# Kernel tuning notes

Hardware: AMD Instinct MI355X
Metric: run time of the kernel (lower is better)

The kernel has to match this reference:

```python
import jax, jax.numpy as jnp
import numpy as np

NIBBLE_SHIFTS = jnp.arange(8, dtype=jnp.int32) * 4


def _unpack_int4(packed):
    # packed: [..., P] int32 -> [..., P*8] int32 values in [0, 15]
    vals = (packed[..., None] >> NIBBLE_SHIFTS) & 0xF
    return vals.reshape(*packed.shape[:-1], packed.shape[-1] * 8)


def setup_inputs() -> dict:
    key = jax.random.key(0)
    k1, k2, k3, k4, k5, k6 = jax.random.split(key, 6)
    M, K, N, G = 4096, 4096, 11008, 128
    inp = jax.random.normal(k1, (M, K), dtype=jnp.float32)
    qweight = jax.random.randint(k2, (K, N // 8), 0, 2147483647, dtype=jnp.int32)
    woq_scales = jax.random.uniform(k3, (K // G, N), dtype=jnp.float32)
    woq_qzeros = jax.random.randint(k4, (K // G, N // 8), 0, 2147483647, dtype=jnp.int32)
    woq_bias = jax.random.normal(k5, (N,), dtype=jnp.float32)
    mul = jax.random.normal(k6, (M, N), dtype=jnp.float32)
    return {"inp": inp, "qweight": qweight, "woq_scales": woq_scales,
            "woq_qzeros": woq_qzeros, "woq_bias": woq_bias, "mul": mul,
            "group_size": G}


def reference(inp, qweight, woq_scales, woq_qzeros, woq_bias, mul, group_size):
    K = qweight.shape[0]
    # dequantize int4 weights: w = (q - z) * scale, per group of `group_size` K-rows
    w_int = _unpack_int4(qweight).astype(jnp.float32)            # [K, N]
    z_int = _unpack_int4(woq_qzeros).astype(jnp.float32)         # [K/G, N]
    zeros_full = jnp.repeat(z_int, group_size, axis=0)           # [K, N]
    scales_full = jnp.repeat(woq_scales, group_size, axis=0)     # [K, N]
    w = (w_int - zeros_full) * scales_full                       # [K, N]
    woq_out = inp @ w + woq_bias                                 # [M, N]
    return jax.nn.silu(woq_out) * mul
```

## Files before the change

### kernel.cpp

```cpp
#include <hip/hip_runtime.h>
#include <hip/hip_bf16.h>

typedef __attribute__((ext_vector_type(8))) short short8;
typedef __attribute__((ext_vector_type(4))) short short4v;
typedef __attribute__((ext_vector_type(4))) float float4v;

__device__ __forceinline__ short f2bf(float f) {
  union { float f; unsigned u; } v; v.f = f;
  unsigned r = v.u + 0x7fffu + ((v.u >> 16) & 1u);
  return (short)(r >> 16);
}

typedef const __attribute__((address_space(1))) unsigned int* as1_u32p;
typedef __attribute__((address_space(3))) unsigned int* as3_u32p;

__device__ __forceinline__ void gl_lds16(const void* g, void* l) {
  __builtin_amdgcn_global_load_lds((as1_u32p)g, (as3_u32p)l, 16, 0, 0);
}

__global__ __launch_bounds__(256, 4)
void prep_kernel(const int* __restrict__ qw,
                 const float* __restrict__ scales,
                 const int* __restrict__ qzeros,
                 short* __restrict__ Bt,
                 const float* __restrict__ inp,
                 short* __restrict__ Abf,
                 int K, int N, int G, int nDq, long long nA)
{
  constexpr int KP = 72;
  __shared__ short Ls[256 * KP];

  if ((int)blockIdx.x >= nDq) {
    const long long i =
        (((long long)blockIdx.x - nDq) * blockDim.x + threadIdx.x) * 8;
    if (i >= nA) return;
    const float4v a = *(const float4v*)(inp + i);
    const float4v b = *(const float4v*)(inp + i + 4);
    short8 h;
    h[0] = f2bf(a[0]); h[1] = f2bf(a[1]); h[2] = f2bf(a[2]); h[3] = f2bf(a[3]);
    h[4] = f2bf(b[0]); h[5] = f2bf(b[1]); h[6] = f2bf(b[2]); h[7] = f2bf(b[3]);
    *(short8*)(Abf + i) = h;
    return;
  }

  const int KB  = K >> 6;
  const int N8  = N >> 3;
  const int k0  = ((int)blockIdx.x % KB) * 64;
  const int nb  = (int)blockIdx.x / KB;
  const int n0  = nb * 256;
  const int n80 = nb * 32;
  const int g   = k0 / G;
  const int t   = threadIdx.x;
  const int kloc = t >> 3;
  const int w4   = (t & 7) * 4;

  const int4 z4 = *(const int4*)(qzeros + (size_t)g * N8 + n80 + w4);
  const int za[4] = {z4.x, z4.y, z4.z, z4.w};
  float sc[32];
  #pragma unroll
  for (int ii = 0; ii < 8; ++ii)
    *(float4v*)(sc + ii * 4) =
        *(const float4v*)(scales + (size_t)g * N + n0 + w4 * 8 + ii * 4);

  #pragma unroll
  for (int kh = 0; kh < 2; ++kh) {
    const int k = kloc + kh * 32;
    const int4 q4 = *(const int4*)(qw + (size_t)(k0 + k) * N8 + n80 + w4);
    const int qa[4] = {q4.x, q4.y, q4.z, q4.w};
    #pragma unroll
    for (int ii = 0; ii < 4; ++ii) {
      #pragma unroll
      for (int j = 0; j < 8; ++j) {
        const float z = (float)((za[ii] >> (4 * j)) & 0xF);
        const float q = (float)((qa[ii] >> (4 * j)) & 0xF);
        Ls[(w4 * 8 + ii * 8 + j) * KP + k] = f2bf((q - z) * sc[ii * 8 + j]);
      }
    }
  }
  __syncthreads();

  #pragma unroll
  for (int it = 0; it < 8; ++it) {
    const int idx = t + it * 256;
    const int row = idx >> 3;
    const int ch  = (idx & 7) * 8;
    const short8 v = *(const short8*)(&Ls[row * KP + ch]);
    *(short8*)(Bt + (size_t)(n0 + row) * K + k0 + ch) = v;
  }
}

__global__ __launch_bounds__(256, 2)
void dequant_kernel_v0(const int* __restrict__ qw,
                       const float* __restrict__ scales,
                       const int* __restrict__ qzeros,
                       short* __restrict__ Bt,
                       int K, int N, int G)
{
  __shared__ short Ls[128 * 64];
  const int N8  = N >> 3;
  const int k0  = blockIdx.x * 64;
  const int n80 = blockIdx.y * 16;
  const int g   = k0 / G;
  const int tid  = threadIdx.x;
  const int lane = tid & 63;
  const int w    = tid >> 6;

  const int4 q4 = *(const int4*)(qw + (size_t)(k0 + lane) * N8 + n80 + w * 4);
  const int4 z4 = *(const int4*)(qzeros + (size_t)g * N8 + n80 + w * 4);
  const int qa[4] = {q4.x, q4.y, q4.z, q4.w};
  const int za[4] = {z4.x, z4.y, z4.z, z4.w};

  #pragma unroll
  for (int it = 0; it < 4; ++it) {
    const int n8l = w * 4 + it;
    const float4v s0 = *(const float4v*)(scales + (size_t)g * N + (n80 + n8l) * 8);
    const float4v s1 = *(const float4v*)(scales + (size_t)g * N + (n80 + n8l) * 8 + 4);
    const float sc[8] = {s0[0], s0[1], s0[2], s0[3], s1[0], s1[1], s1[2], s1[3]};
    const int wq = qa[it], wz = za[it];
    #pragma unroll
    for (int j = 0; j < 8; ++j) {
      const float z = (float)((wz >> (4 * j)) & 0xF);
      const float q = (float)((wq >> (4 * j)) & 0xF);
      Ls[(n8l * 8 + j) * 64 + lane] = f2bf((q - z) * sc[j]);
    }
  }
  __syncthreads();

  #pragma unroll
  for (int it = 0; it < 4; ++it) {
    const int c   = tid + it * 256;
    const int row = c >> 3;
    const int off = (c & 7) * 8;
    const short8 v = *(const short8*)(&Ls[row * 64 + off]);
    *(short8*)(Bt + (size_t)(n80 * 8 + row) * K + k0 + off) = v;
  }
}

__global__ __launch_bounds__(256, 4)
void aconv_kernel(const float* __restrict__ in, short* __restrict__ out, long long n)
{
  const long long i = ((long long)blockIdx.x * blockDim.x + threadIdx.x) * 8;
  if (i >= n) return;
  const float4v a = *(const float4v*)(in + i);
  const float4v b = *(const float4v*)(in + i + 4);
  short8 h;
  h[0] = f2bf(a[0]); h[1] = f2bf(a[1]); h[2] = f2bf(a[2]); h[3] = f2bf(a[3]);
  h[4] = f2bf(b[0]); h[5] = f2bf(b[1]); h[6] = f2bf(b[2]); h[7] = f2bf(b[3]);
  *(short8*)(out + i) = h;
}

__global__ __launch_bounds__(512, 2)
void gemm256_silu_mul_kernel(const short* __restrict__ A,
                             const short* __restrict__ Bt,
                             const float* __restrict__ bias,
                             const float* __restrict__ mulp,
                             float*       __restrict__ out,
                             int M, int N, int K)
{
  __shared__ short L[2][2][16384];

  const int tid  = threadIdx.x;
  const int lane = tid & 63;
  const int wave = tid >> 6;
  const int wm   = wave >> 2;
  const int wn   = wave & 3;

  const int nwg = gridDim.x;
  const int q8 = nwg >> 3, r8 = nwg & 7;
  const int xcd = blockIdx.x & 7, sub = blockIdx.x >> 3;
  const int swz = (xcd < r8 ? xcd * (q8 + 1) : r8 * (q8 + 1) + (xcd - r8) * q8) + sub;
  const int nbx = N >> 8;
  const int bx = swz % nbx, by = swz / nbx;
  const int m0 = by << 8, n0 = bx << 8;

  const short* Ab = A  + (size_t)m0 * K;
  const short* Bb = Bt + (size_t)n0 * K;

  const int srow = lane >> 2;
  const int scol = (((lane & 3) ^ ((lane & 32) >> 4))) * 8;
  const int fm = lane & 15;
  const int ko = ((lane >> 4) * 8) ^ ((fm & 8) ? 16 : 0);

  const int BG0 = wave * 2;
  const int BG1 = wave * 2 + 1;
  const int AEg = (wave & 3) + (wave >> 2) * 8;
  const int ALg = AEg + 4;

  float4v acc[8][4];
  #pragma unroll
  for (int i = 0; i < 8; ++i)
    #pragma unroll
    for (int j = 0; j < 4; ++j)
      acc[i][j] = (float4v){0.f, 0.f, 0.f, 0.f};

  const int NT = K >> 6;

  auto stage2 = [&](int buf, int ab, int g, const short* __restrict__ base, int kk) {
    #pragma unroll
    for (int ks = 0; ks < 2; ++ks)
      gl_lds16(base + (size_t)(g * 16 + srow) * K + kk + ks * 32 + scol,
               &L[buf][ab][(g * 2 + ks) * 512]);
  };

  stage2(0, 0, AEg, Ab, 0);
  stage2(0, 1, BG0, Bb, 0);
  stage2(0, 1, BG1, Bb, 0);
  stage2(0, 0, ALg, Ab, 0);
  if (NT > 1) {
    stage2(1, 0, AEg, Ab, 64);
    stage2(1, 1, BG0, Bb, 64);
    stage2(1, 1, BG1, Bb, 64);
    asm volatile("s_waitcnt vmcnt(10)" ::: "memory");
  } else {
    asm volatile("s_waitcnt vmcnt(4)" ::: "memory");
  }
  __builtin_amdgcn_s_barrier();

  for (int t = 0; t < NT; ++t) {
    const int cur = t & 1;
    const int nxt = cur ^ 1;
    const bool i1 = (t + 1) < NT;
    const bool i2 = (t + 2) < NT;
    const int kk1 = (t + 1) << 6;
    const int kk2 = (t + 2) << 6;

    short8 af[4][2], bf[4][2];

    #pragma unroll
    for (int i = 0; i < 4; ++i)
      #pragma unroll
      for (int ks = 0; ks < 2; ++ks)
        af[i][ks] = *(const short8*)(
            &L[cur][0][((wm * 8 + i) * 2 + ks) * 512 + fm * 32 + ko]);
    #pragma unroll
    for (int j = 0; j < 4; j += 2)
      #pragma unroll
      for (int ks = 0; ks < 2; ++ks)
        bf[j][ks] = *(const short8*)(
            &L[cur][1][((wn * 4 + j) * 2 + ks) * 512 + fm * 32 + ko]);
    if (i1) stage2(nxt, 0, ALg, Ab, kk1);
    __builtin_amdgcn_s_barrier();
    asm volatile("s_waitcnt lgkmcnt(0)");
    __builtin_amdgcn_s_setprio(1);
    #pragma unroll
    for (int i = 0; i < 4; ++i)
      #pragma unroll
      for (int j = 0; j < 4; j += 2)
        #pragma unroll
        for (int ks = 0; ks < 2; ++ks)
          acc[i][j] = __builtin_amdgcn_mfma_f32_16x16x32_bf16(
              af[i][ks], bf[j][ks], acc[i][j], 0, 0, 0);
    __builtin_amdgcn_s_setprio(0);
    if (i1) { asm volatile("s_waitcnt vmcnt(10)" ::: "memory"); }
    else    { asm volatile("s_waitcnt vmcnt(2)"  ::: "memory"); }
    __builtin_amdgcn_s_barrier();

    #pragma unroll
    for (int j = 1; j < 4; j += 2)
      #pragma unroll
      for (int ks = 0; ks < 2; ++ks)
        bf[j][ks] = *(const short8*)(
            &L[cur][1][((wn * 4 + j) * 2 + ks) * 512 + fm * 32 + ko]);
    if (i2) stage2(cur, 0, AEg, Ab, kk2);
    __builtin_amdgcn_s_barrier();
    asm volatile("s_waitcnt lgkmcnt(0)");
    __builtin_amdgcn_s_setprio(1);
    #pragma unroll
    for (int i = 0; i < 4; ++i)
      #pragma unroll
      for (int j = 1; j < 4; j += 2)
        #pragma unroll
        for (int ks = 0; ks < 2; ++ks)
          acc[i][j] = __builtin_amdgcn_mfma_f32_16x16x32_bf16(
              af[i][ks], bf[j][ks], acc[i][j], 0, 0, 0);
    __builtin_amdgcn_s_setprio(0);
    if (i2)      { asm volatile("s_waitcnt vmcnt(10)" ::: "memory"); }
    else if (i1) { asm volatile("s_waitcnt vmcnt(8)"  ::: "memory"); }
    else         { asm volatile("s_waitcnt vmcnt(0)"  ::: "memory"); }
    __builtin_amdgcn_s_barrier();

    #pragma unroll
    for (int i = 0; i < 4; ++i)
      #pragma unroll
      for (int ks = 0; ks < 2; ++ks)
        af[i][ks] = *(const short8*)(
            &L[cur][0][((wm * 8 + 4 + i) * 2 + ks) * 512 + fm * 32 + ko]);
    if (i2) stage2(cur, 1, BG0, Bb, kk2);
    __builtin_amdgcn_s_barrier();
    asm volatile("s_waitcnt lgkmcnt(0)");
    __builtin_amdgcn_s_setprio(1);
    #pragma unroll
    for (int i = 0; i < 4; ++i)
      #pragma unroll
      for (int j = 0; j < 4; j += 2)
        #pragma unroll
        for (int ks = 0; ks < 2; ++ks)
          acc[4 + i][j] = __builtin_amdgcn_mfma_f32_16x16x32_bf16(
              af[i][ks], bf[j][ks], acc[4 + i][j], 0, 0, 0);
    __builtin_amdgcn_s_setprio(0);
    __builtin_amdgcn_s_barrier();

    if (i2) stage2(cur, 1, BG1, Bb, kk2);
    __builtin_amdgcn_s_barrier();
    __builtin_amdgcn_s_setprio(1);
    #pragma unroll
    for (int i = 0; i < 4; ++i)
      #pragma unroll
      for (int j = 1; j < 4; j += 2)
        #pragma unroll
        for (int ks = 0; ks < 2; ++ks)
          acc[4 + i][j] = __builtin_amdgcn_mfma_f32_16x16x32_bf16(
              af[i][ks], bf[j][ks], acc[4 + i][j], 0, 0, 0);
    __builtin_amdgcn_s_setprio(0);
    if (i2)      { asm volatile("s_waitcnt vmcnt(10)" ::: "memory"); }
    else if (i1) { asm volatile("s_waitcnt vmcnt(4)"  ::: "memory"); }
    __builtin_amdgcn_s_barrier();
  }

  const int cn  = lane & 15;
  const int cr4 = (lane >> 4) * 4;
  #pragma unroll
  for (int mt = 0; mt < 8; ++mt) {
    #pragma unroll
    for (int nt = 0; nt < 4; ++nt) {
      const int n  = n0 + wn * 64 + nt * 16 + cn;
      const float bn = bias[n];
      #pragma unroll
      for (int i = 0; i < 4; ++i) {
        const int m = m0 + wm * 128 + mt * 16 + cr4 + i;
        float x = acc[mt][nt][i] + bn;
        float s = x / (1.0f + __expf(-x));
        out[(size_t)m * N + n] = s * mulp[(size_t)m * N + n];
      }
    }
  }
}

__global__ __launch_bounds__(256, 2)
void gemm_silu_mul_kernel(const short* __restrict__ A,
                          const short* __restrict__ Bt,
                          const float* __restrict__ bias,
                          const float* __restrict__ mulp,
                          float*       __restrict__ out,
                          int M, int N, int K)
{
  __shared__ short As[128 * 64];
  __shared__ short Bs[128 * 64];

  const int tid  = threadIdx.x;
  const int lane = tid & 63;
  const int wave = tid >> 6;
  const int wr = (wave >> 1) * 64;
  const int wc = (wave & 1) * 64;
  const int m0 = blockIdx.y * 128;
  const int n0 = blockIdx.x * 128;

  float4v acc[4][4];
  #pragma unroll
  for (int i = 0; i < 4; ++i)
    #pragma unroll
    for (int j = 0; j < 4; ++j)
      acc[i][j] = (float4v){0.f, 0.f, 0.f, 0.f};

  const int fm = lane & 15;
  const int fk = (lane >> 4) * 8;
  const int srow = lane >> 3;
  const int scol = (lane & 7) * 8;

  for (int k0 = 0; k0 < K; k0 += 64) {
    #pragma unroll
    for (int c = 0; c < 4; ++c) {
      const int chunk = wave * 4 + c;
      const int row   = chunk * 8 + srow;
      gl_lds16(A  + (size_t)(m0 + row) * K + k0 + scol, &As[chunk * 512]);
      gl_lds16(Bt + (size_t)(n0 + row) * K + k0 + scol, &Bs[chunk * 512]);
    }
    __syncthreads();

    #pragma unroll
    for (int ks = 0; ks < 64; ks += 32) {
      short8 a[4], b[4];
      #pragma unroll
      for (int mt = 0; mt < 4; ++mt)
        a[mt] = *(const short8*)(&As[(wr + mt * 16 + fm) * 64 + ks + fk]);
      #pragma unroll
      for (int nt = 0; nt < 4; ++nt)
        b[nt] = *(const short8*)(&Bs[(wc + nt * 16 + fm) * 64 + ks + fk]);
      #pragma unroll
      for (int mt = 0; mt < 4; ++mt)
        #pragma unroll
        for (int nt = 0; nt < 4; ++nt)
          acc[mt][nt] = __builtin_amdgcn_mfma_f32_16x16x32_bf16(a[mt], b[nt], acc[mt][nt], 0, 0, 0);
    }
    __syncthreads();
  }

  const int cn = lane & 15;
  const int cr = (lane >> 4) * 4;
  #pragma unroll
  for (int mt = 0; mt < 4; ++mt) {
    #pragma unroll
    for (int nt = 0; nt < 4; ++nt) {
      const int n  = n0 + wc + nt * 16 + cn;
      const float bn = bias[n];
      #pragma unroll
      for (int i = 0; i < 4; ++i) {
        const int m = m0 + wr + mt * 16 + cr + i;
        float x = acc[mt][nt][i] + bn;
        float s = x / (1.0f + __expf(-x));
        out[(size_t)m * N + n] = s * mulp[(size_t)m * N + n];
      }
    }
  }
}

#define BM 128
#define BN 128
#define BK 64
#define LDA 72
#define LDB 72

__global__ __launch_bounds__(256, 2)
void woq_silu_mul_kernel(const float* __restrict__ inp, const int* __restrict__ qw,
                         const float* __restrict__ scales, const int* __restrict__ qzeros,
                         const float* __restrict__ bias, const float* __restrict__ mulp,
                         float* __restrict__ out, int M, int N, int K, int G)
{
  __shared__ short As[BM * LDA];
  __shared__ short Bs[BN * LDB];
  const int tid  = threadIdx.x;
  const int lane = tid & 63;
  const int wave = tid >> 6;
  const int wr = (wave >> 1) * 64;
  const int wc = (wave & 1) * 64;
  const int m0 = blockIdx.y * BM;
  const int n0 = blockIdx.x * BN;
  const int N8 = N >> 3;
  float4v acc[4][4];
  #pragma unroll
  for (int i = 0; i < 4; ++i)
    #pragma unroll
    for (int j = 0; j < 4; ++j)
      acc[i][j] = (float4v){0.f, 0.f, 0.f, 0.f};
  const int n8l  = tid >> 4;
  const int kloc = (tid & 15) * 4;
  const int fm = lane & 15;
  const int fk = (lane >> 4) * 8;
  for (int k0 = 0; k0 < K; k0 += BK) {
    #pragma unroll
    for (int i = 0; i < 8; ++i) {
      int f = tid + i * 256;
      int row = f >> 4;
      int col = (f & 15) * 4;
      float4v a4 = *(const float4v*)(inp + (size_t)(m0 + row) * K + k0 + col);
      short4v h;
      h[0] = f2bf(a4[0]); h[1] = f2bf(a4[1]); h[2] = f2bf(a4[2]); h[3] = f2bf(a4[3]);
      *(short4v*)(&As[row * LDA + col]) = h;
    }
    {
      const int g = k0 / G;
      const int n8g = (n0 >> 3) + n8l;
      const int zw = qzeros[(size_t)g * N8 + n8g];
      const float4v s0 = *(const float4v*)(scales + (size_t)g * N + n0 + n8l * 8);
      const float4v s1 = *(const float4v*)(scales + (size_t)g * N + n0 + n8l * 8 + 4);
      float sc[8] = {s0[0], s0[1], s0[2], s0[3], s1[0], s1[1], s1[2], s1[3]};
      int w[4];
      #pragma unroll
      for (int kk = 0; kk < 4; ++kk)
        w[kk] = qw[(size_t)(k0 + kloc + kk) * N8 + n8g];
      #pragma unroll
      for (int j = 0; j < 8; ++j) {
        const float zj = (float)((zw >> (4 * j)) & 0xF);
        const float sj = sc[j];
        short4v h;
        #pragma unroll
        for (int kk = 0; kk < 4; ++kk) {
          int q = (w[kk] >> (4 * j)) & 0xF;
          h[kk] = f2bf(((float)q - zj) * sj);
        }
        *(short4v*)(&Bs[(n8l * 8 + j) * LDB + kloc]) = h;
      }
    }
    __syncthreads();
    #pragma unroll
    for (int ks = 0; ks < BK; ks += 32) {
      short8 a[4], b[4];
      #pragma unroll
      for (int mt = 0; mt < 4; ++mt)
        a[mt] = *(const short8*)(&As[(wr + mt * 16 + fm) * LDA + ks + fk]);
      #pragma unroll
      for (int nt = 0; nt < 4; ++nt)
        b[nt] = *(const short8*)(&Bs[(wc + nt * 16 + fm) * LDB + ks + fk]);
      #pragma unroll
      for (int mt = 0; mt < 4; ++mt)
        #pragma unroll
        for (int nt = 0; nt < 4; ++nt)
          acc[mt][nt] = __builtin_amdgcn_mfma_f32_16x16x32_bf16(a[mt], b[nt], acc[mt][nt], 0, 0, 0);
    }
    __syncthreads();
  }
  const int cn = lane & 15;
  const int cr = (lane >> 4) * 4;
  #pragma unroll
  for (int mt = 0; mt < 4; ++mt) {
    #pragma unroll
    for (int nt = 0; nt < 4; ++nt) {
      const int n = n0 + wc + nt * 16 + cn;
      const float bn = bias[n];
      #pragma unroll
      for (int i = 0; i < 4; ++i) {
        const int m = m0 + wr + mt * 16 + cr + i;
        float x = acc[mt][nt][i] + bn;
        float s = x / (1.0f + __expf(-x));
        out[(size_t)m * N + n] = s * mulp[(size_t)m * N + n];
      }
    }
  }
}

extern "C" void kernel_launch(void* const* d_in, const int* in_sizes, int n_in,
                              void* d_out, int out_size, void* d_ws, size_t ws_size,
                              hipStream_t stream) {
  const float* inp    = (const float*)d_in[0];
  const int*   qw     = (const int*)d_in[1];
  const float* scales = (const float*)d_in[2];
  const int*   qzeros = (const int*)d_in[3];
  const float* bias   = (const float*)d_in[4];
  const float* mulp   = (const float*)d_in[5];
  float*       out    = (float*)d_out;

  const int N = in_sizes[4];
  const int K = (int)(((long long)in_sizes[1] * 8) / N);
  const int M = (int)((long long)in_sizes[0] / K);
  const int G = K / (in_sizes[2] / N);

  const size_t btBytes = (size_t)N * K * sizeof(short);
  const size_t aBytes  = (size_t)M * K * sizeof(short);

  if (ws_size >= btBytes + aBytes) {
    short* Bt  = (short*)d_ws;
    short* Abf = (short*)((char*)d_ws + btBytes);
    const long long nA = (long long)M * K;

    const bool dqOk = (N & 255) == 0 && (K & 63) == 0 && G >= 64 && (G & 63) == 0
                      && (nA & 7) == 0;
    if (dqOk) {
      const int nDq = (K / 64) * (N / 256);
      const int nAc = (int)((nA / 8 + 255) / 256);
      prep_kernel<<<dim3((unsigned)(nDq + nAc)), dim3(256), 0, stream>>>(
          qw, scales, qzeros, Bt, inp, Abf, K, N, G, nDq, nA);
    } else {
      dim3 dq_grid(K / 64, (N / 8) / 16);
      dequant_kernel_v0<<<dq_grid, dim3(256), 0, stream>>>(qw, scales, qzeros, Bt, K, N, G);
      aconv_kernel<<<dim3((unsigned)((nA / 8 + 255) / 256)), dim3(256), 0, stream>>>(inp, Abf, nA);
    }

    if ((M & 255) == 0 && (N & 255) == 0 && (K & 63) == 0) {
      dim3 grid((unsigned)((N >> 8) * (M >> 8)));
      gemm256_silu_mul_kernel<<<grid, dim3(512), 0, stream>>>(Abf, Bt, bias, mulp, out, M, N, K);
    } else {
      dim3 grid(N / 128, M / 128);
      gemm_silu_mul_kernel<<<grid, dim3(256), 0, stream>>>(Abf, Bt, bias, mulp, out, M, N, K);
    }
  } else {
    dim3 grid(N / BN, M / BM);
    woq_silu_mul_kernel<<<grid, dim3(256), 0, stream>>>(inp, qw, scales, qzeros,
                                                        bias, mulp, out, M, N, K, G);
  }
}
```

Before: 698.0 us.

## Software-pipeline LDS fragment loads across iterations and drop lgkmcnt waits

```diff
diff --git a/kernel.cpp b/kernel.cpp
--- a/kernel.cpp
+++ b/kernel.cpp
@@ -202,18 +202,30 @@
                &L[buf][ab][(g * 2 + ks) * 512]);
   };
 
+  short8 afE[4][2], afL[4][2], bfE[2][2], bfO[2][2];
+
   stage2(0, 0, AEg, Ab, 0);
   stage2(0, 1, BG0, Bb, 0);
   stage2(0, 1, BG1, Bb, 0);
   stage2(0, 0, ALg, Ab, 0);
-  if (NT > 1) {
-    stage2(1, 0, AEg, Ab, 64);
-    stage2(1, 1, BG0, Bb, 64);
-    stage2(1, 1, BG1, Bb, 64);
-    asm volatile("s_waitcnt vmcnt(10)" ::: "memory");
-  } else {
-    asm volatile("s_waitcnt vmcnt(4)" ::: "memory");
-  }
+  stage2(1, 0, AEg, Ab, 64);
+  stage2(1, 1, BG0, Bb, 64);
+  asm volatile("s_waitcnt vmcnt(8)" ::: "memory");
+  __builtin_amdgcn_s_barrier();
+  #pragma unroll
+  for (int i = 0; i < 4; ++i)
+    #pragma unroll
+    for (int ks = 0; ks < 2; ++ks)
+      afE[i][ks] = *(const short8*)(
+          &L[0][0][((wm * 8 + i) * 2 + ks) * 512 + fm * 32 + ko]);
+  #pragma unroll
+  for (int jj = 0; jj < 2; ++jj)
+    #pragma unroll
+    for (int ks = 0; ks < 2; ++ks)
+      bfE[jj][ks] = *(const short8*)(
+          &L[0][1][((wn * 4 + jj * 2) * 2 + ks) * 512 + fm * 32 + ko]);
+  stage2(1, 1, BG1, Bb, 64);
+  asm volatile("s_waitcnt vmcnt(8)" ::: "memory");
   __builtin_amdgcn_s_barrier();
 
   for (int t = 0; t < NT; ++t) {
@@ -224,96 +236,92 @@
     const int kk1 = (t + 1) << 6;
     const int kk2 = (t + 2) << 6;
 
-    short8 af[4][2], bf[4][2];
-
+    #pragma unroll
+    for (int jj = 0; jj < 2; ++jj)
+      #pragma unroll
+      for (int ks = 0; ks < 2; ++ks)
+        bfO[jj][ks] = *(const short8*)(
+            &L[cur][1][((wn * 4 + jj * 2 + 1) * 2 + ks) * 512 + fm * 32 + ko]);
+    if (i1) stage2(nxt, 0, ALg, Ab, kk1);
+    __builtin_amdgcn_s_barrier();
+    __builtin_amdgcn_s_setprio(1);
     #pragma unroll
     for (int i = 0; i < 4; ++i)
       #pragma unroll
+      for (int jj = 0; jj < 2; ++jj)
+        #pragma unroll
+        for (int ks = 0; ks < 2; ++ks)
+          acc[i][jj * 2] = __builtin_amdgcn_mfma_f32_16x16x32_bf16(
+              afE[i][ks], bfE[jj][ks], acc[i][jj * 2], 0, 0, 0);
+    __builtin_amdgcn_s_setprio(0);
+    if (i1) { asm volatile("s_waitcnt vmcnt(8)" ::: "memory"); }
+    else    { asm volatile("s_waitcnt vmcnt(0)" ::: "memory"); }
+    __builtin_amdgcn_s_barrier();
+
+    #pragma unroll
+    for (int i = 0; i < 4; ++i)
+      #pragma unroll
       for (int ks = 0; ks < 2; ++ks)
-        af[i][ks] = *(const short8*)(
-            &L[cur][0][((wm * 8 + i) * 2 + ks) * 512 + fm * 32 + ko]);
-    #pragma unroll
-    for (int j = 0; j < 4; j += 2)
-      #pragma unroll
-      for (int ks = 0; ks < 2; ++ks)
-        bf[j][ks] = *(const short8*)(
-            &L[cur][1][((wn * 4 + j) * 2 + ks) * 512 + fm * 32 + ko]);
-    if (i1) stage2(nxt, 0, ALg, Ab, kk1);
-    __builtin_amdgcn_s_barrier();
-    asm volatile("s_waitcnt lgkmcnt(0)");
+        afL[i][ks] = *(const short8*)(
+            &L[cur][0][((wm * 8 + 4 + i) * 2 + ks) * 512 + fm * 32 + ko]);
+    if (i2) stage2(cur, 0, AEg, Ab, kk2);
+    __builtin_amdgcn_s_barrier();
     __builtin_amdgcn_s_setprio(1);
     #pragma unroll
     for (int i = 0; i < 4; ++i)
       #pragma unroll
-      for (int j = 0; j < 4; j += 2)
+      for (int jj = 0; jj < 2; ++jj)
         #pragma unroll
         for (int ks = 0; ks < 2; ++ks)
-          acc[i][j] = __builtin_amdgcn_mfma_f32_16x16x32_bf16(
-              af[i][ks], bf[j][ks], acc[i][j], 0, 0, 0);
+          acc[i][jj * 2 + 1] = __builtin_amdgcn_mfma_f32_16x16x32_bf16(
+              afE[i][ks], bfO[jj][ks], acc[i][jj * 2 + 1], 0, 0, 0);
     __builtin_amdgcn_s_setprio(0);
-    if (i1) { asm volatile("s_waitcnt vmcnt(10)" ::: "memory"); }
-    else    { asm volatile("s_waitcnt vmcnt(2)"  ::: "memory"); }
-    __builtin_amdgcn_s_barrier();
-
-    #pragma unroll
-    for (int j = 1; j < 4; j += 2)
-      #pragma unroll
-      for (int ks = 0; ks < 2; ++ks)
-        bf[j][ks] = *(const short8*)(
-            &L[cur][1][((wn * 4 + j) * 2 + ks) * 512 + fm * 32 + ko]);
-    if (i2) stage2(cur, 0, AEg, Ab, kk2);
-    __builtin_amdgcn_s_barrier();
-    asm volatile("s_waitcnt lgkmcnt(0)");
+    __builtin_amdgcn_s_barrier();
+
+    if (i2) stage2(cur, 1, BG0, Bb, kk2);
+    __builtin_amdgcn_s_barrier();
     __builtin_amdgcn_s_setprio(1);
     #pragma unroll
     for (int i = 0; i < 4; ++i)
       #pragma unroll
-      for (int j = 1; j < 4; j += 2)
+      for (int jj = 0; jj < 2; ++jj)
         #pragma unroll
         for (int ks = 0; ks < 2; ++ks)
-          acc[i][j] = __builtin_amdgcn_mfma_f32_16x16x32_bf16(
-              af[i][ks], bf[j][ks], acc[i][j], 0, 0, 0);
+          acc[4 + i][jj * 2] = __builtin_amdgcn_mfma_f32_16x16x32_bf16(
+              afL[i][ks], bfE[jj][ks], acc[4 + i][jj * 2], 0, 0, 0);
     __builtin_amdgcn_s_setprio(0);
-    if (i2)      { asm volatile("s_waitcnt vmcnt(10)" ::: "memory"); }
-    else if (i1) { asm volatile("s_waitcnt vmcnt(8)"  ::: "memory"); }
-    else         { asm volatile("s_waitcnt vmcnt(0)"  ::: "memory"); }
-    __builtin_amdgcn_s_barrier();
-
+    if (i2)      { asm volatile("s_waitcnt vmcnt(8)" ::: "memory"); }
+    else if (i1) { asm volatile("s_waitcnt vmcnt(4)" ::: "memory"); }
+    __builtin_amdgcn_s_barrier();
+
+    if (i1) {
+      #pragma unroll
+      for (int i = 0; i < 4; ++i)
+        #pragma unroll
+        for (int ks = 0; ks < 2; ++ks)
+          afE[i][ks] = *(const short8*)(
+              &L[nxt][0][((wm * 8 + i) * 2 + ks) * 512 + fm * 32 + ko]);
+      #pragma unroll
+      for (int jj = 0; jj < 2; ++jj)
+        #pragma unroll
+        for (int ks = 0; ks < 2; ++ks)
+          bfE[jj][ks] = *(const short8*)(
+              &L[nxt][1][((wn * 4 + jj * 2) * 2 + ks) * 512 + fm * 32 + ko]);
+    }
+    if (i2) stage2(cur, 1, BG1, Bb, kk2);
+    __builtin_amdgcn_s_barrier();
+    __builtin_amdgcn_s_setprio(1);
     #pragma unroll
     for (int i = 0; i < 4; ++i)
       #pragma unroll
-      for (int ks = 0; ks < 2; ++ks)
-        af[i][ks] = *(const short8*)(
-            &L[cur][0][((wm * 8 + 4 + i) * 2 + ks) * 512 + fm * 32 + ko]);
-    if (i2) stage2(cur, 1, BG0, Bb, kk2);
-    __builtin_amdgcn_s_barrier();
-    asm volatile("s_waitcnt lgkmcnt(0)");
-    __builtin_amdgcn_s_setprio(1);
-    #pragma unroll
-    for (int i = 0; i < 4; ++i)
-      #pragma unroll
-      for (int j = 0; j < 4; j += 2)
+      for (int jj = 0; jj < 2; ++jj)
         #pragma unroll
         for (int ks = 0; ks < 2; ++ks)
-          acc[4 + i][j] = __builtin_amdgcn_mfma_f32_16x16x32_bf16(
-              af[i][ks], bf[j][ks], acc[4 + i][j], 0, 0, 0);
+          acc[4 + i][jj * 2 + 1] = __builtin_amdgcn_mfma_f32_16x16x32_bf16(
+              afL[i][ks], bfO[jj][ks], acc[4 + i][jj * 2 + 1], 0, 0, 0);
     __builtin_amdgcn_s_setprio(0);
-    __builtin_amdgcn_s_barrier();
-
-    if (i2) stage2(cur, 1, BG1, Bb, kk2);
-    __builtin_amdgcn_s_barrier();
-    __builtin_amdgcn_s_setprio(1);
-    #pragma unroll
-    for (int i = 0; i < 4; ++i)
-      #pragma unroll
-      for (int j = 1; j < 4; j += 2)
-        #pragma unroll
-        for (int ks = 0; ks < 2; ++ks)
-          acc[4 + i][j] = __builtin_amdgcn_mfma_f32_16x16x32_bf16(
-              af[i][ks], bf[j][ks], acc[4 + i][j], 0, 0, 0);
-    __builtin_amdgcn_s_setprio(0);
-    if (i2)      { asm volatile("s_waitcnt vmcnt(10)" ::: "memory"); }
-    else if (i1) { asm volatile("s_waitcnt vmcnt(4)"  ::: "memory"); }
+    if (i2)      { asm volatile("s_waitcnt vmcnt(8)" ::: "memory"); }
+    else if (i1) { asm volatile("s_waitcnt vmcnt(2)" ::: "memory"); }
     __builtin_amdgcn_s_barrier();
   }
 
@@ -555,7 +563,7 @@
       aconv_kernel<<<dim3((unsigned)((nA / 8 + 255) / 256)), dim3(256), 0, stream>>>(inp, Abf, nA);
     }
 
-    if ((M & 255) == 0 && (N & 255) == 0 && (K & 63) == 0) {
+    if ((M & 255) == 0 && (N & 255) == 0 && (K & 63) == 0 && K >= 128) {
       dim3 grid((unsigned)((N >> 8) * (M >> 8)));
       gemm256_silu_mul_kernel<<<grid, dim3(512), 0, stream>>>(Abf, Bt, bias, mulp, out, M, N, K);
     } else {
```

Result: no change. 702.1 us (+0.6%).
